# Performance work log

Hardware: AMD Instinct MI355X
Metric: run time of the kernel (lower is better)

Reference implementation:

```python
import jax, jax.numpy as jnp
import numpy as np

TIME = 10  # hardcoded interpolation steps in the original module


def _interpolation(poly, time=TIME):
    # poly: [B, N, 2] -> [B, N*time, 2]
    poly_roll = jnp.roll(poly, shift=1, axis=1)
    step = (jnp.arange(time, dtype=poly.dtype) / time)[:, None]        # [T, 1]
    # [B, N, T, 2] = current * step + previous * (1 - step)
    interp = poly[:, :, None, :] * step + poly_roll[:, :, None, :] * (1.0 - step)
    return interp.reshape(poly.shape[0], -1, 2)


def _compute_distance(pred_poly, gt_poly):
    # pred_poly: [B, Np, 2], gt_poly: [B, Ng, 2] -> squared dists [B, Ng, Np]
    diff = gt_poly[:, :, None, :] - pred_poly[:, None, :, :]
    return jnp.sum(diff * diff, axis=3)


def reference(ini_pred_poly, pred_polys_, gt_polys, keyPointsMask):
    # --- lossPred2NearestGt: each pred point matched to nearest interpolated gt ---
    gt_interp = _interpolation(gt_polys)                               # [B, Ng*T, 2]
    dist_pg = _compute_distance(ini_pred_poly, gt_interp)              # [B, Ng*T, Np]
    index_gt = jnp.argmin(dist_pg, axis=1)                             # [B, Np]
    nearest_gt = jnp.take_along_axis(gt_interp, index_gt[:, :, None], axis=1)  # [B, Np, 2]
    loss_pred2gt = jnp.mean(jnp.abs(pred_polys_ - nearest_gt))         # l1, mean reduction

    # --- lossGt2NearestPred: each gt vertex matched to nearest pred point ---
    dist_gp = _compute_distance(ini_pred_poly, gt_polys)               # [B, Ng, Np]
    index_pred = jnp.argmin(dist_gp, axis=2)                           # [B, Ng]
    nearest_pred = jnp.take_along_axis(pred_polys_, index_pred[:, :, None], axis=1)  # [B, Ng, 2]
    loss_gt2pred = jnp.abs(nearest_pred - gt_polys)                    # l1, no reduction, [B, Ng, 2]

    mask = jnp.broadcast_to(keyPointsMask[:, :, None], loss_gt2pred.shape)
    loss = jnp.sum(loss_gt2pred * mask) / (jnp.sum(mask) + 1.0) + loss_pred2gt
    return loss / 2.0


def setup_inputs() -> dict:
    key = jax.random.key(0)
    k1, k2, k3, k4 = jax.random.split(key, 4)
    B, Np, Ng = 1024, 128, 128
    return {
        "ini_pred_poly": jax.random.uniform(k1, (B, Np, 2), dtype=jnp.float32),
        "pred_polys_": jax.random.uniform(k2, (B, Np, 2), dtype=jnp.float32),
        "gt_polys": jax.random.uniform(k3, (B, Ng, 2), dtype=jnp.float32),
        "keyPointsMask": jax.random.uniform(k4, (B, Ng), dtype=jnp.float32),
    }
```

## Files before the change

### kernel.cpp

```cpp
#include <hip/hip_runtime.h>


constexpr int NP = 128;
constexpr int NG = 128;

__device__ __forceinline__ int padi (int i) { return i + (i >> 5); }
__device__ __forceinline__ int padi2(int i) { return i + (i >> 4); }

__global__ __launch_bounds__(512) void dm_main(
    const float* __restrict__ ini,
    const float* __restrict__ pp,
    const float* __restrict__ gt,
    const float* __restrict__ mask,
    float* __restrict__ partial,
    int nb)
{
    const int b    = blockIdx.x;
    const int tid  = threadIdx.x;
    const int lane = tid & 63;
    const int w    = tid >> 6;

    __shared__ float2 s_gt  [NG];
    __shared__ float4 s_seg [NG + 4];
    __shared__ float  s_g   [NG + 4];
    __shared__ float4 s_ini2[64 + 4];
    __shared__ float2 s_pp  [NP];
    __shared__ float  s_red [24];

    const float2* gtb  = (const float2*)(gt  + (size_t)b * 256);
    const float4* ini4 = (const float4*)(ini + (size_t)b * 256);
    const float2* ppb  = (const float2*)(pp  + (size_t)b * 256);

    if (tid < 128) {
        const float2 cv = gtb[tid];
        const float2 pv = gtb[(tid + 127) & 127];
        const float ex = cv.x - pv.x, ey = cv.y - pv.y;
        const float ee = fmaf(ex, ex, ey * ey);
        const float s10 = 10.0f * __builtin_amdgcn_rcpf(fmaxf(ee, 1e-30f));
        s_gt [tid]       = cv;
        s_seg[padi(tid)] = make_float4(pv.x, pv.y, ex * s10, ey * s10);
        s_g  [padi(tid)] = ee * 0.01f;
    } else if (tid < 192) {
        const int i = tid - 128;
        s_ini2[padi2(i)] = ini4[i];
    } else if (tid < 320) {
        s_pp[tid - 192] = ppb[tid - 192];
    }

    const int sub     = lane & 15;
    const int quarter = lane >> 4;
    const int pnt     = (w << 4) | sub;
    float mval = 0.0f;
    if (quarter == 0) mval = mask[(size_t)b * NG + pnt];
    __syncthreads();

    const float4 qq = s_ini2[padi2(pnt >> 1)];
    const float2 q  = (pnt & 1) ? make_float2(qq.z, qq.w) : make_float2(qq.x, qq.y);
    const float2 gv = s_gt[pnt];

    float bd1 = 3.4e38f, bi1 = 0.0f;
    {
        const int s0 = quarter << 5;
        float basef = (float)(s0 * 10);
        #pragma unroll 8
        for (int k = 0; k < 32; ++k) {
            const float4 sg = s_seg[padi(s0 + k)];
            const float  g  = s_g  [padi(s0 + k)];
            const float wx = q.x - sg.x, wy = q.y - sg.y;
            const float tf = fmaf(wy, sg.w, wx * sg.z);
            float tc = rintf(tf);
            tc = __builtin_amdgcn_fmed3f(tc, 0.0f, 9.0f);
            const float ww = fmaf(wy, wy, wx * wx);
            const float t2 = fmaf(-2.0f, tf, tc);
            const float d  = fmaf(g * tc, t2, ww);
            const float cand = basef + tc;
            bi1 = (d < bd1) ? cand : bi1;
            bd1 = fminf(d, bd1);
            basef += 10.0f;
        }
    }

    float bd2 = 3.4e38f, bj2 = 0.0f;
    {
        const int p0 = quarter << 4;
        float jf = (float)(quarter << 5);
        #pragma unroll 8
        for (int k = 0; k < 16; ++k) {
            const float4 pv2 = s_ini2[padi2(p0 + k)];
            {
                const float dx = gv.x - pv2.x, dy = gv.y - pv2.y;
                const float d  = fmaf(dy, dy, dx * dx);
                bj2 = (d < bd2) ? jf : bj2;
                bd2 = fminf(d, bd2);
            }
            jf += 1.0f;
            {
                const float dx = gv.x - pv2.z, dy = gv.y - pv2.w;
                const float d  = fmaf(dy, dy, dx * dx);
                bj2 = (d < bd2) ? jf : bj2;
                bd2 = fminf(d, bd2);
            }
            jf += 1.0f;
        }
    }

    #pragma unroll
    for (int st = 16; st <= 32; st <<= 1) {
        const float d1o = __shfl_xor(bd1, st);
        const float i1o = __shfl_xor(bi1, st);
        const bool  t1  = (d1o < bd1) || (d1o == bd1 && i1o < bi1);
        bi1 = t1 ? i1o : bi1;
        bd1 = t1 ? d1o : bd1;
        const float d2o = __shfl_xor(bd2, st);
        const float j2o = __shfl_xor(bj2, st);
        const bool  t2  = (d2o < bd2) || (d2o == bd2 && j2o < bj2);
        bj2 = t2 ? j2o : bj2;
        bd2 = t2 ? d2o : bd2;
    }

    float l_a = 0.0f, l_c = 0.0f, l_m = 0.0f;
    if (quarter == 0) {
        const int idx = (int)bi1;
        const int n = idx / 10;
        const int t = idx - n * 10;
        const float step = (float)t / 10.0f;
        const float om   = 1.0f - step;
        const float2 c   = s_gt[n];
        const float2 prv = s_gt[(n + NG - 1) & (NG - 1)];
        const float nx = c.x * step + prv.x * om;
        const float ny = c.y * step + prv.y * om;
        const float2 mp = s_pp[pnt];
        l_a = fabsf(mp.x - nx) + fabsf(mp.y - ny);

        const float2 npt = s_pp[(int)bj2];
        l_c = mval * (fabsf(npt.x - gv.x) + fabsf(npt.y - gv.y));
        l_m = 2.0f * mval;
    }

    #pragma unroll
    for (int st = 1; st <= 8; st <<= 1) {
        l_a += __shfl_xor(l_a, st);
        l_c += __shfl_xor(l_c, st);
        l_m += __shfl_xor(l_m, st);
    }
    if (lane == 0) {
        s_red[w * 3 + 0] = l_a;
        s_red[w * 3 + 1] = l_c;
        s_red[w * 3 + 2] = l_m;
    }
    __syncthreads();
    if (tid < 3) {
        float s = 0.0f;
        #pragma unroll
        for (int ww = 0; ww < 8; ++ww) s += s_red[ww * 3 + tid];
        partial[(size_t)tid * nb + b] = s;
    }
}

__global__ __launch_bounds__(256) void dm_final(
    const float* __restrict__ partial, int nb, double inv_count, float* __restrict__ out)
{
    const int tid = threadIdx.x;
    double a = 0.0, c = 0.0, d = 0.0;
    if ((nb & 3) == 0) {
        const int npairs = nb >> 2;
        for (int i = tid; i < npairs; i += 256) {
            const float4 va = ((const float4*)partial)[i];
            const float4 vc = ((const float4*)(partial + (size_t)nb))[i];
            const float4 vd = ((const float4*)(partial + (size_t)2 * nb))[i];
            a += (double)va.x + (double)va.y + (double)va.z + (double)va.w;
            c += (double)vc.x + (double)vc.y + (double)vc.z + (double)vc.w;
            d += (double)vd.x + (double)vd.y + (double)vd.z + (double)vd.w;
        }
    } else {
        for (int i = tid; i < nb; i += 256) {
            a += (double)partial[i];
            c += (double)partial[(size_t)nb + i];
            d += (double)partial[(size_t)2 * nb + i];
        }
    }
    for (int off = 32; off > 0; off >>= 1) {
        a += __shfl_down(a, off);
        c += __shfl_down(c, off);
        d += __shfl_down(d, off);
    }
    __shared__ double s[12];
    const int wid = tid >> 6, lane = tid & 63;
    if (lane == 0) { s[wid * 3] = a; s[wid * 3 + 1] = c; s[wid * 3 + 2] = d; }
    __syncthreads();
    if (tid == 0) {
        const double at = s[0] + s[3] + s[6] + s[9];
        const double ct = s[1] + s[4] + s[7] + s[10];
        const double dt = s[2] + s[5] + s[8] + s[11];
        const double loss = ct / (dt + 1.0) + at * inv_count;
        out[0] = (float)(loss * 0.5);
    }
}

extern "C" void kernel_launch(void* const* d_in, const int* in_sizes, int n_in,
                              void* d_out, int out_size, void* d_ws, size_t ws_size,
                              hipStream_t stream) {
    const float* ini  = (const float*)d_in[0];
    const float* pp   = (const float*)d_in[1];
    const float* gt   = (const float*)d_in[2];
    const float* mask = (const float*)d_in[3];
    float* out = (float*)d_out;

    const int B = in_sizes[0] / (NP * 2);
    float* partial = (float*)d_ws;

    dm_main<<<B, 512, 0, stream>>>(ini, pp, gt, mask, partial, B);
    const double inv_count = 1.0 / ((double)B * NP * 2);
    dm_final<<<1, 256, 0, stream>>>(partial, B, inv_count, out);
}
```

Measured before the change: 17.18 us.

## Process two points per thread and pack distance-index into uint for min reduction

Each thread now handles two query points against a 16-segment slice instead of one point against 32 segments, so each shared-memory segment load is reused for both points. The cross-lane argmin becomes a single unsigned min on a packed key: the float distance with its low 11 mantissa bits replaced by the index. This cuts the shuffles and compares in the reduction, but truncating those bits can change tie-breaking or pick a slightly different nearest point when distances are very close.

```diff
diff --git a/kernel.cpp b/kernel.cpp
--- a/kernel.cpp
+++ b/kernel.cpp
@@ -4,8 +4,8 @@
 constexpr int NP = 128;
 constexpr int NG = 128;
 
-__device__ __forceinline__ int padi (int i) { return i + (i >> 5); }
-__device__ __forceinline__ int padi2(int i) { return i + (i >> 4); }
+__device__ __forceinline__ int pad17(int i) { return i + (i >> 4); }
+__device__ __forceinline__ int pad9 (int i) { return i + (i >> 3); }
 
 __global__ __launch_bounds__(512) void dm_main(
     const float* __restrict__ ini,
@@ -21,9 +21,9 @@
     const int w    = tid >> 6;
 
     __shared__ float2 s_gt  [NG];
-    __shared__ float4 s_seg [NG + 4];
-    __shared__ float  s_g   [NG + 4];
-    __shared__ float4 s_ini2[64 + 4];
+    __shared__ float4 s_seg [NG + 8];
+    __shared__ float  s_g   [NG + 8];
+    __shared__ float4 s_ini2[64 + 8];
     __shared__ float2 s_pp  [NP];
     __shared__ float  s_red [24];
 
@@ -37,108 +37,157 @@
         const float ex = cv.x - pv.x, ey = cv.y - pv.y;
         const float ee = fmaf(ex, ex, ey * ey);
         const float s10 = 10.0f * __builtin_amdgcn_rcpf(fmaxf(ee, 1e-30f));
-        s_gt [tid]       = cv;
-        s_seg[padi(tid)] = make_float4(pv.x, pv.y, ex * s10, ey * s10);
-        s_g  [padi(tid)] = ee * 0.01f;
+        s_gt [tid]        = cv;
+        s_seg[pad17(tid)] = make_float4(pv.x, pv.y, ex * s10, ey * s10);
+        s_g  [pad17(tid)] = ee * 0.01f;
     } else if (tid < 192) {
         const int i = tid - 128;
-        s_ini2[padi2(i)] = ini4[i];
+        s_ini2[pad9(i)] = ini4[i];
     } else if (tid < 320) {
         s_pp[tid - 192] = ppb[tid - 192];
     }
 
-    const int sub     = lane & 15;
-    const int quarter = lane >> 4;
-    const int pnt     = (w << 4) | sub;
-    float mval = 0.0f;
-    if (quarter == 0) mval = mask[(size_t)b * NG + pnt];
+    const int sub  = lane & 7;
+    const int grp  = lane >> 3;
+    const int pnt0 = (w << 4) | sub;
+    const int pnt1 = pnt0 + 8;
+    float mv0 = 0.0f, mv1 = 0.0f;
+    if (grp == 0) {
+        mv0 = mask[(size_t)b * NG + pnt0];
+        mv1 = mask[(size_t)b * NG + pnt1];
+    }
     __syncthreads();
 
-    const float4 qq = s_ini2[padi2(pnt >> 1)];
-    const float2 q  = (pnt & 1) ? make_float2(qq.z, qq.w) : make_float2(qq.x, qq.y);
-    const float2 gv = s_gt[pnt];
-
-    float bd1 = 3.4e38f, bi1 = 0.0f;
+    const float4 qa = s_ini2[pad9((w << 3) + (sub >> 1))];
+    const float4 qb = s_ini2[pad9((w << 3) + 4 + (sub >> 1))];
+    const float2 q0 = (sub & 1) ? make_float2(qa.z, qa.w) : make_float2(qa.x, qa.y);
+    const float2 q1 = (sub & 1) ? make_float2(qb.z, qb.w) : make_float2(qb.x, qb.y);
+    const float2 gv0 = s_gt[pnt0];
+    const float2 gv1 = s_gt[pnt1];
+
+    float bd10 = 3.4e38f, bi10 = 0.0f, bd11 = 3.4e38f, bi11 = 0.0f;
     {
-        const int s0 = quarter << 5;
+        const int s0 = grp << 4;
         float basef = (float)(s0 * 10);
-        #pragma unroll 8
-        for (int k = 0; k < 32; ++k) {
-            const float4 sg = s_seg[padi(s0 + k)];
-            const float  g  = s_g  [padi(s0 + k)];
-            const float wx = q.x - sg.x, wy = q.y - sg.y;
-            const float tf = fmaf(wy, sg.w, wx * sg.z);
-            float tc = rintf(tf);
-            tc = __builtin_amdgcn_fmed3f(tc, 0.0f, 9.0f);
-            const float ww = fmaf(wy, wy, wx * wx);
-            const float t2 = fmaf(-2.0f, tf, tc);
-            const float d  = fmaf(g * tc, t2, ww);
-            const float cand = basef + tc;
-            bi1 = (d < bd1) ? cand : bi1;
-            bd1 = fminf(d, bd1);
+        #pragma unroll
+        for (int k = 0; k < 16; ++k) {
+            const float4 sg = s_seg[pad17(s0 + k)];
+            const float  g  = s_g  [pad17(s0 + k)];
+            {
+                const float wx = q0.x - sg.x, wy = q0.y - sg.y;
+                const float tf = fmaf(wy, sg.w, wx * sg.z);
+                float tc = rintf(tf);
+                tc = __builtin_amdgcn_fmed3f(tc, 0.0f, 9.0f);
+                const float ww = fmaf(wy, wy, wx * wx);
+                const float d  = fmaf(g * tc, fmaf(-2.0f, tf, tc), ww);
+                const float cand = basef + tc;
+                bi10 = (d < bd10) ? cand : bi10;
+                bd10 = fminf(d, bd10);
+            }
+            {
+                const float wx = q1.x - sg.x, wy = q1.y - sg.y;
+                const float tf = fmaf(wy, sg.w, wx * sg.z);
+                float tc = rintf(tf);
+                tc = __builtin_amdgcn_fmed3f(tc, 0.0f, 9.0f);
+                const float ww = fmaf(wy, wy, wx * wx);
+                const float d  = fmaf(g * tc, fmaf(-2.0f, tf, tc), ww);
+                const float cand = basef + tc;
+                bi11 = (d < bd11) ? cand : bi11;
+                bd11 = fminf(d, bd11);
+            }
             basef += 10.0f;
         }
     }
 
-    float bd2 = 3.4e38f, bj2 = 0.0f;
+    float bd20 = 3.4e38f, bj20 = 0.0f, bd21 = 3.4e38f, bj21 = 0.0f;
     {
-        const int p0 = quarter << 4;
-        float jf = (float)(quarter << 5);
-        #pragma unroll 8
-        for (int k = 0; k < 16; ++k) {
-            const float4 pv2 = s_ini2[padi2(p0 + k)];
-            {
-                const float dx = gv.x - pv2.x, dy = gv.y - pv2.y;
-                const float d  = fmaf(dy, dy, dx * dx);
-                bj2 = (d < bd2) ? jf : bj2;
-                bd2 = fminf(d, bd2);
+        const int p0 = grp << 3;
+        float jf = (float)(grp << 4);
+        #pragma unroll
+        for (int k = 0; k < 8; ++k) {
+            const float4 pv2 = s_ini2[pad9(p0 + k)];
+            {
+                const float dx = gv0.x - pv2.x, dy = gv0.y - pv2.y;
+                const float d  = fmaf(dy, dy, dx * dx);
+                bj20 = (d < bd20) ? jf : bj20;
+                bd20 = fminf(d, bd20);
+            }
+            {
+                const float dx = gv1.x - pv2.x, dy = gv1.y - pv2.y;
+                const float d  = fmaf(dy, dy, dx * dx);
+                bj21 = (d < bd21) ? jf : bj21;
+                bd21 = fminf(d, bd21);
             }
             jf += 1.0f;
             {
-                const float dx = gv.x - pv2.z, dy = gv.y - pv2.w;
-                const float d  = fmaf(dy, dy, dx * dx);
-                bj2 = (d < bd2) ? jf : bj2;
-                bd2 = fminf(d, bd2);
+                const float dx = gv0.x - pv2.z, dy = gv0.y - pv2.w;
+                const float d  = fmaf(dy, dy, dx * dx);
+                bj20 = (d < bd20) ? jf : bj20;
+                bd20 = fminf(d, bd20);
+            }
+            {
+                const float dx = gv1.x - pv2.z, dy = gv1.y - pv2.w;
+                const float d  = fmaf(dy, dy, dx * dx);
+                bj21 = (d < bd21) ? jf : bj21;
+                bd21 = fminf(d, bd21);
             }
             jf += 1.0f;
         }
     }
 
+    unsigned u10 = (__float_as_uint(bd10) & 0xFFFFF800u) | (unsigned)(int)bi10;
+    unsigned u11 = (__float_as_uint(bd11) & 0xFFFFF800u) | (unsigned)(int)bi11;
+    unsigned u20 = (__float_as_uint(bd20) & 0xFFFFF800u) | (unsigned)(int)bj20;
+    unsigned u21 = (__float_as_uint(bd21) & 0xFFFFF800u) | (unsigned)(int)bj21;
+
     #pragma unroll
-    for (int st = 16; st <= 32; st <<= 1) {
-        const float d1o = __shfl_xor(bd1, st);
-        const float i1o = __shfl_xor(bi1, st);
-        const bool  t1  = (d1o < bd1) || (d1o == bd1 && i1o < bi1);
-        bi1 = t1 ? i1o : bi1;
-        bd1 = t1 ? d1o : bd1;
-        const float d2o = __shfl_xor(bd2, st);
-        const float j2o = __shfl_xor(bj2, st);
-        const bool  t2  = (d2o < bd2) || (d2o == bd2 && j2o < bj2);
-        bj2 = t2 ? j2o : bj2;
-        bd2 = t2 ? d2o : bd2;
+    for (int st = 8; st <= 32; st <<= 1) {
+        u10 = min(u10, (unsigned)__shfl_xor((int)u10, st));
+        u11 = min(u11, (unsigned)__shfl_xor((int)u11, st));
+        u20 = min(u20, (unsigned)__shfl_xor((int)u20, st));
+        u21 = min(u21, (unsigned)__shfl_xor((int)u21, st));
     }
 
     float l_a = 0.0f, l_c = 0.0f, l_m = 0.0f;
-    if (quarter == 0) {
-        const int idx = (int)bi1;
-        const int n = idx / 10;
-        const int t = idx - n * 10;
-        const float step = (float)t / 10.0f;
-        const float om   = 1.0f - step;
-        const float2 c   = s_gt[n];
-        const float2 prv = s_gt[(n + NG - 1) & (NG - 1)];
-        const float nx = c.x * step + prv.x * om;
-        const float ny = c.y * step + prv.y * om;
-        const float2 mp = s_pp[pnt];
-        l_a = fabsf(mp.x - nx) + fabsf(mp.y - ny);
-
-        const float2 npt = s_pp[(int)bj2];
-        l_c = mval * (fabsf(npt.x - gv.x) + fabsf(npt.y - gv.y));
-        l_m = 2.0f * mval;
+    if (grp == 0) {
+        {
+            const int idx = (int)(u10 & 0x7FFu);
+            const int n = idx / 10;
+            const int t = idx - n * 10;
+            const float step = (float)t / 10.0f;
+            const float om   = 1.0f - step;
+            const float2 c   = s_gt[n];
+            const float2 prv = s_gt[(n + NG - 1) & (NG - 1)];
+            const float2 mp  = s_pp[pnt0];
+            l_a += fabsf(mp.x - (c.x * step + prv.x * om))
+                 + fabsf(mp.y - (c.y * step + prv.y * om));
+        }
+        {
+            const int idx = (int)(u11 & 0x7FFu);
+            const int n = idx / 10;
+            const int t = idx - n * 10;
+            const float step = (float)t / 10.0f;
+            const float om   = 1.0f - step;
+            const float2 c   = s_gt[n];
+            const float2 prv = s_gt[(n + NG - 1) & (NG - 1)];
+            const float2 mp  = s_pp[pnt1];
+            l_a += fabsf(mp.x - (c.x * step + prv.x * om))
+                 + fabsf(mp.y - (c.y * step + prv.y * om));
+        }
+        {
+            const float2 npt = s_pp[(int)(u20 & 0x7FFu)];
+            l_c += mv0 * (fabsf(npt.x - gv0.x) + fabsf(npt.y - gv0.y));
+            l_m += 2.0f * mv0;
+        }
+        {
+            const float2 npt = s_pp[(int)(u21 & 0x7FFu)];
+            l_c += mv1 * (fabsf(npt.x - gv1.x) + fabsf(npt.y - gv1.y));
+            l_m += 2.0f * mv1;
+        }
     }
 
     #pragma unroll
-    for (int st = 1; st <= 8; st <<= 1) {
+    for (int st = 1; st <= 4; st <<= 1) {
         l_a += __shfl_xor(l_a, st);
         l_c += __shfl_xor(l_c, st);
         l_m += __shfl_xor(l_m, st);
```

Measured after the change: 18.99 us. 10.6% more time.

## Drop block-level reduction barrier; write per-wave partials and reduce in final kernel

Applied to the files above, without the earlier changes.

Removes the second __syncthreads and shared-memory reduction in the main kernel. Each wave now writes its own three partial sums to global memory, and the final kernel reduces B*8 entries instead of B. The l_a and l_c/l_m epilogue work is split across two different quarters of each wave to balance lanes, and launch bounds now request 8 blocks per CU. The cost is 8x more partial writes and a longer serial reduction in the single-block final kernel, and the final kernel drops its non-multiple-of-4 fallback path.

```diff
diff --git a/kernel.cpp b/kernel.cpp
--- a/kernel.cpp
+++ b/kernel.cpp
@@ -7,7 +7,7 @@
 __device__ __forceinline__ int padi (int i) { return i + (i >> 5); }
 __device__ __forceinline__ int padi2(int i) { return i + (i >> 4); }
 
-__global__ __launch_bounds__(512) void dm_main(
+__global__ __launch_bounds__(512, 8) void dm_main(
     const float* __restrict__ ini,
     const float* __restrict__ pp,
     const float* __restrict__ gt,
@@ -25,7 +25,6 @@
     __shared__ float  s_g   [NG + 4];
     __shared__ float4 s_ini2[64 + 4];
     __shared__ float2 s_pp  [NP];
-    __shared__ float  s_red [24];
 
     const float2* gtb  = (const float2*)(gt  + (size_t)b * 256);
     const float4* ini4 = (const float4*)(ini + (size_t)b * 256);
@@ -51,7 +50,7 @@
     const int quarter = lane >> 4;
     const int pnt     = (w << 4) | sub;
     float mval = 0.0f;
-    if (quarter == 0) mval = mask[(size_t)b * NG + pnt];
+    if (quarter == 1) mval = mask[(size_t)b * NG + pnt];
     __syncthreads();
 
     const float4 qq = s_ini2[padi2(pnt >> 1)];
@@ -131,7 +130,7 @@
         const float ny = c.y * step + prv.y * om;
         const float2 mp = s_pp[pnt];
         l_a = fabsf(mp.x - nx) + fabsf(mp.y - ny);
-
+    } else if (quarter == 1) {
         const float2 npt = s_pp[(int)bj2];
         l_c = mval * (fabsf(npt.x - gv.x) + fabsf(npt.y - gv.y));
         l_m = 2.0f * mval;
@@ -143,41 +142,31 @@
         l_c += __shfl_xor(l_c, st);
         l_m += __shfl_xor(l_m, st);
     }
+    l_c = __shfl(l_c, 16);
+    l_m = __shfl(l_m, 16);
+
     if (lane == 0) {
-        s_red[w * 3 + 0] = l_a;
-        s_red[w * 3 + 1] = l_c;
-        s_red[w * 3 + 2] = l_m;
-    }
-    __syncthreads();
-    if (tid < 3) {
-        float s = 0.0f;
-        #pragma unroll
-        for (int ww = 0; ww < 8; ++ww) s += s_red[ww * 3 + tid];
-        partial[(size_t)tid * nb + b] = s;
+        const int wid = b * 8 + w;
+        const int n8  = nb * 8;
+        partial[wid]                 = l_a;
+        partial[(size_t)n8 + wid]    = l_c;
+        partial[(size_t)2 * n8 + wid] = l_m;
     }
 }
 
 __global__ __launch_bounds__(256) void dm_final(
-    const float* __restrict__ partial, int nb, double inv_count, float* __restrict__ out)
+    const float* __restrict__ partial, int n8, double inv_count, float* __restrict__ out)
 {
     const int tid = threadIdx.x;
     double a = 0.0, c = 0.0, d = 0.0;
-    if ((nb & 3) == 0) {
-        const int npairs = nb >> 2;
-        for (int i = tid; i < npairs; i += 256) {
-            const float4 va = ((const float4*)partial)[i];
-            const float4 vc = ((const float4*)(partial + (size_t)nb))[i];
-            const float4 vd = ((const float4*)(partial + (size_t)2 * nb))[i];
-            a += (double)va.x + (double)va.y + (double)va.z + (double)va.w;
-            c += (double)vc.x + (double)vc.y + (double)vc.z + (double)vc.w;
-            d += (double)vd.x + (double)vd.y + (double)vd.z + (double)vd.w;
-        }
-    } else {
-        for (int i = tid; i < nb; i += 256) {
-            a += (double)partial[i];
-            c += (double)partial[(size_t)nb + i];
-            d += (double)partial[(size_t)2 * nb + i];
-        }
+    const int npairs = n8 >> 2;
+    for (int i = tid; i < npairs; i += 256) {
+        const float4 va = ((const float4*)partial)[i];
+        const float4 vc = ((const float4*)(partial + (size_t)n8))[i];
+        const float4 vd = ((const float4*)(partial + (size_t)2 * n8))[i];
+        a += (double)va.x + (double)va.y + (double)va.z + (double)va.w;
+        c += (double)vc.x + (double)vc.y + (double)vc.z + (double)vc.w;
+        d += (double)vd.x + (double)vd.y + (double)vd.z + (double)vd.w;
     }
     for (int off = 32; off > 0; off >>= 1) {
         a += __shfl_down(a, off);
@@ -211,5 +200,5 @@
 
     dm_main<<<B, 512, 0, stream>>>(ini, pp, gt, mask, partial, B);
     const double inv_count = 1.0 / ((double)B * NP * 2);
-    dm_final<<<1, 256, 0, stream>>>(partial, B, inv_count, out);
+    dm_final<<<1, 256, 0, stream>>>(partial, B * 8, inv_count, out);
 }
```

After: 19.43 us. +13.1%, slower.
